# Optimization experiments

Measured on AMD Instinct MI355X. Metric: run time of the kernel, lower is better.

Reference implementation:

```python
import jax, jax.numpy as jnp
import numpy as np

C = 96          # channels (= output_dim)
NUM_HEADS = 6
DILS = (1, 2, 3)
KS_ATT = 3      # dilate-attention kernel size
KS_COR = 5      # self-correlation kernel size
PAD_COR = 2
LN_EPS = 1e-5


def _unfold(x, k, dil, pad):
    # torch.nn.Unfold(kernel=k, dilation=dil, padding=pad, stride=1)
    # x: [B, C, H, W] -> [B, C, k*k, H, W] (channel-major, kernel row-major)
    B, c, H, W = x.shape
    xp = jnp.pad(x, ((0, 0), (0, 0), (pad, pad), (pad, pad)))
    patches = [xp[:, :, i * dil:i * dil + H, j * dil:j * dil + W]
               for i in range(k) for j in range(k)]
    return jnp.stack(patches, axis=2)


def _layernorm(x, g, b):
    m = jnp.mean(x, axis=-1, keepdims=True)
    v = jnp.mean((x - m) ** 2, axis=-1, keepdims=True)
    return (x - m) * jax.lax.rsqrt(v + LN_EPS) * g + b


def _dilate_attn(q, k, v, dil, head_dim, scale):
    # q,k,v: [B, cb, H, W] with cb = C // num_dilation
    B, cb, H, W = q.shape
    heads = cb // head_dim
    qf = q.reshape(B, heads, head_dim, H * W)                                  # bhdn
    kp = _unfold(k, KS_ATT, dil, dil).reshape(B, heads, head_dim, KS_ATT * KS_ATT, H * W)
    attn = jax.nn.softmax(jnp.einsum('bhdn,bhdkn->bhnk', qf, kp) * scale, axis=-1)
    vp = _unfold(v, KS_ATT, dil, dil).reshape(B, heads, head_dim, KS_ATT * KS_ATT, H * W)
    out = jnp.einsum('bhnk,bhdkn->bnhd', attn, vp)                             # [B,HW,heads,hd]
    return out.reshape(B, H, W, cb)


def _forward(x, g1, b1, Wqkv, bqkv, Wproj, bproj, g2, b2, W1, bm1, W2, bm2):
    B, Cc, H, W = x.shape
    nd = len(DILS)
    head_dim = Cc // NUM_HEADS
    scale = head_dim ** (-0.5)

    xh = jnp.transpose(x, (0, 2, 3, 1))                                        # [B,H,W,C]

    # --- MultiDilatelocalAttention block ---
    y = _layernorm(xh, g1, b1)
    qkv = jnp.einsum('bhwc,oc->bhwo', y, Wqkv) + bqkv                          # 1x1 conv == linear
    qkv = jnp.transpose(qkv, (0, 3, 1, 2)).reshape(B, 3, nd, Cc // nd, H, W)
    outs = []
    for i, d in enumerate(DILS):
        outs.append(_dilate_attn(qkv[:, 0, i], qkv[:, 1, i], qkv[:, 2, i], d, head_dim, scale))
    a = jnp.concatenate(outs, axis=-1)                                         # dilation-major channels
    a = a @ Wproj.T + bproj
    xh = xh + a

    # --- MLP block ---
    z = _layernorm(xh, g2, b2)
    z = jax.nn.gelu(z @ W1.T + bm1, approximate=False) @ W2.T + bm2
    xh = xh + z

    # --- self-correlation ---
    xc = jnp.transpose(xh, (0, 3, 1, 2))                                       # [B,C,H,W]
    xc = jax.nn.relu(xc)
    nrm = jnp.sqrt(jnp.sum(xc * xc, axis=1, keepdims=True))
    xc = xc / jnp.maximum(nrm, 1e-12)                                          # F.normalize dim=1
    pat = _unfold(xc, KS_COR, 1, PAD_COR)                                      # [B,C,25,H,W]
    out = pat.reshape(B, Cc, KS_COR, KS_COR, H, W) * xc[:, :, None, None]
    return jnp.transpose(out, (0, 1, 4, 5, 2, 3))                              # [B,C,H,W,5,5]


def setup_inputs() -> dict:
    key = jax.random.key(0)
    ks = jax.random.split(key, 8)
    B, H, W = 8, 64, 64
    s = 0.02
    return {
        'x': jax.random.normal(ks[0], (B, C, H, W), jnp.float32),
        'g1': jnp.ones((C,), jnp.float32),
        'b1': jnp.zeros((C,), jnp.float32),
        'Wqkv': jax.random.normal(ks[1], (3 * C, C), jnp.float32) * s,
        'bqkv': jnp.zeros((3 * C,), jnp.float32),
        'Wproj': jax.random.normal(ks[2], (C, C), jnp.float32) * s,
        'bproj': jnp.zeros((C,), jnp.float32),
        'g2': jnp.ones((C,), jnp.float32),
        'b2': jnp.zeros((C,), jnp.float32),
        'W1': jax.random.normal(ks[3], (4 * C, C), jnp.float32) * s,
        'bm1': jnp.zeros((4 * C,), jnp.float32),
        'W2': jax.random.normal(ks[4], (C, 4 * C), jnp.float32) * s,
        'bm2': jnp.zeros((C,), jnp.float32),
    }


def reference(x, g1, b1, Wqkv, bqkv, Wproj, bproj, g2, b2, W1, bm1, W2, bm2):
    return _forward(x, g1, b1, Wqkv, bqkv, Wproj, bproj, g2, b2, W1, bm1, W2, bm2)
```

## Files before the change

### kernel.cpp

```cpp
#include <hip/hip_runtime.h>
#include <math.h>

#define NN 4096
#define BN 32768

using short8 = __attribute__((ext_vector_type(8))) short;
using f32x4  = __attribute__((ext_vector_type(4))) float;
typedef unsigned short ushort_t;

__device__ inline ushort_t f2bf(float f) {
    unsigned u = __builtin_bit_cast(unsigned, f);
    u += 0x7FFFu + ((u >> 16) & 1u);
    return (ushort_t)(u >> 16);
}
__device__ inline float bflo(unsigned u) {
    return __builtin_bit_cast(float, u << 16);
}
__device__ inline float bfhi(unsigned u) {
    return __builtin_bit_cast(float, u & 0xFFFF0000u);
}
__device__ inline float bf2f(ushort_t h) {
    return __builtin_bit_cast(float, ((unsigned)h) << 16);
}

__global__ __launch_bounds__(256) void k0_cvt(
    const float* __restrict__ Wqkv, const float* __restrict__ Wproj,
    const float* __restrict__ W1, const float* __restrict__ W2,
    ushort_t* __restrict__ wb)
{
    int i = blockIdx.x * 256 + threadIdx.x;
    float v;
    if (i < 27648)      v = Wqkv[i];
    else if (i < 36864) v = Wproj[i - 27648];
    else if (i < 73728) v = W1[i - 36864];
    else                v = W2[i - 73728];
    wb[i] = f2bf(v);
}

__global__ __launch_bounds__(256) void k1_ln_qkv(
    const float* __restrict__ x, const float* __restrict__ g1, const float* __restrict__ b1,
    const ushort_t* __restrict__ wqkv_b, const float* __restrict__ bqkv,
    unsigned* __restrict__ qkvt32)
{
    __shared__ __align__(16) float    Cs[96 * 69];
    __shared__ __align__(16) ushort_t As[64 * 104];
    __shared__ __align__(16) ushort_t Bs[96 * 104];
    const int tid = threadIdx.x;
    const long bn0 = (long)blockIdx.x * 64;
    const int b = (int)(bn0 >> 12);
    const int n0 = (int)(bn0 & 4095);
    const unsigned* wqkv32 = (const unsigned*)wqkv_b;

    for (int i = 0; i < 24; ++i) {
        int idx = i * 256 + tid;
        int c = idx >> 6, p = idx & 63;
        Cs[c * 69 + p] = x[((long)(b * 96 + c) << 12) + n0 + p];
    }
    __syncthreads();
    {
        int p = tid >> 2, part = tid & 3, c0 = part * 24;
        float s = 0.f, ss = 0.f;
        for (int c = c0; c < c0 + 24; ++c) { float v = Cs[c*69 + p]; s += v; ss += v*v; }
        s  += __shfl_xor(s, 1);  s  += __shfl_xor(s, 2);
        ss += __shfl_xor(ss, 1); ss += __shfl_xor(ss, 2);
        float m = s * (1.f/96.f);
        float rstd = rsqrtf(ss * (1.f/96.f) - m*m + 1e-5f);
        for (int c = c0; c < c0 + 24; ++c)
            Cs[c*69 + p] = (Cs[c*69 + p] - m) * rstd * g1[c] + b1[c];
    }
    __syncthreads();
    for (int i = 0; i < 12; ++i) {
        int idx = i * 256 + tid;
        int p = idx / 48, cp = idx % 48;
        unsigned lo = f2bf(Cs[(2*cp  )*69 + p]);
        unsigned hi = f2bf(Cs[(2*cp+1)*69 + p]);
        *(unsigned*)&As[p * 104 + 2*cp] = lo | (hi << 16);
    }

    const int lane = tid & 63, wv = tid >> 6;
    const int ln = lane & 15, qd = lane >> 4;
    for (int ch = 0; ch < 3; ++ch) {
        __syncthreads();
        for (int i = 0; i < 18; ++i) {
            int idx = i * 256 + tid;
            int o = idx / 48, cp = idx % 48;
            *(unsigned*)&Bs[o * 104 + 2*cp] = wqkv32[(ch*96 + o)*48 + cp];
        }
        __syncthreads();
        f32x4 acc[6];
        #pragma unroll
        for (int t = 0; t < 6; ++t) acc[t] = (f32x4){0.f, 0.f, 0.f, 0.f};
        #pragma unroll
        for (int kc = 0; kc < 3; ++kc) {
            short8 a = *(const short8*)&As[(wv*16 + ln)*104 + kc*32 + qd*8];
            #pragma unroll
            for (int t = 0; t < 6; ++t) {
                short8 bf = *(const short8*)&Bs[(t*16 + ln)*104 + kc*32 + qd*8];
                acc[t] = __builtin_amdgcn_mfma_f32_16x16x32_bf16(a, bf, acc[t], 0, 0, 0);
            }
        }
        #pragma unroll
        for (int t = 0; t < 6; ++t)
            #pragma unroll
            for (int r = 0; r < 4; ++r)
                Cs[(t*16 + ln)*69 + (wv*16 + qd*4 + r)] = acc[t][r];
        __syncthreads();
        for (int i = 0; i < 12; ++i) {
            int idx = i * 256 + tid;
            int cp = idx / 64, p = idx % 64;
            int c = 2*cp;
            float b0v = bqkv[ch*96 + c], b1v = bqkv[ch*96 + c + 1];
            unsigned lo = f2bf(Cs[c*69 + p] + b0v);
            unsigned hi = f2bf(Cs[(c+1)*69 + p] + b1v);
            qkvt32[((long)(b*144 + ch*48 + cp) << 12) + n0 + p] = lo | (hi << 16);
        }
    }
}

__global__ __launch_bounds__(256) void k2_attn(
    const unsigned* __restrict__ qkvt32, unsigned* __restrict__ abt32)
{
    int t = blockIdx.x * 256 + threadIdx.x;
    int n = t & 4095;
    int r = t >> 12;
    int head = r & 1;
    int di = (r >> 1) % 3;
    int b = r / 6;
    int h = n >> 6, w = n & 63;
    int dil = di + 1;
    const int cp0 = di*16 + head*8;
    const unsigned* Q = qkvt32 + ((long)(b*144 +      cp0) << 12);
    const unsigned* K = qkvt32 + ((long)(b*144 + 48 + cp0) << 12);
    const unsigned* V = qkvt32 + ((long)(b*144 + 96 + cp0) << 12);

    float q[16];
    #pragma unroll
    for (int j = 0; j < 8; ++j) {
        unsigned u = Q[((long)j << 12) + n];
        q[2*j] = bflo(u); q[2*j+1] = bfhi(u);
    }

    float logits[9];
    #pragma unroll
    for (int ki = 0; ki < 3; ++ki)
        #pragma unroll
        for (int kj = 0; kj < 3; ++kj) {
            int hh = h + (ki-1)*dil, ww = w + (kj-1)*dil;
            float l = 0.f;
            if ((unsigned)hh < 64u && (unsigned)ww < 64u) {
                int nn = (hh << 6) + ww;
                #pragma unroll
                for (int j = 0; j < 8; ++j) {
                    unsigned u = K[((long)j << 12) + nn];
                    l += q[2*j] * bflo(u) + q[2*j+1] * bfhi(u);
                }
            }
            logits[ki*3 + kj] = l * 0.25f;
        }
    float m = logits[0];
    #pragma unroll
    for (int k = 1; k < 9; ++k) m = fmaxf(m, logits[k]);
    float e[9], s = 0.f;
    #pragma unroll
    for (int k = 0; k < 9; ++k) { e[k] = expf(logits[k] - m); s += e[k]; }
    float inv = 1.f / s;

    float o[16];
    #pragma unroll
    for (int d = 0; d < 16; ++d) o[d] = 0.f;
    #pragma unroll
    for (int ki = 0; ki < 3; ++ki)
        #pragma unroll
        for (int kj = 0; kj < 3; ++kj) {
            int hh = h + (ki-1)*dil, ww = w + (kj-1)*dil;
            if ((unsigned)hh < 64u && (unsigned)ww < 64u) {
                int nn = (hh << 6) + ww;
                float wgt = e[ki*3 + kj] * inv;
                #pragma unroll
                for (int j = 0; j < 8; ++j) {
                    unsigned u = V[((long)j << 12) + nn];
                    o[2*j]   += wgt * bflo(u);
                    o[2*j+1] += wgt * bfhi(u);
                }
            }
        }
    #pragma unroll
    for (int j = 0; j < 8; ++j) {
        unsigned lo = f2bf(o[2*j]), hi = f2bf(o[2*j+1]);
        abt32[((long)(b*48 + cp0 + j) << 12) + n] = lo | (hi << 16);
    }
}

__global__ __launch_bounds__(256) void k345(
    const unsigned* __restrict__ abt32, const float* __restrict__ x,
    const ushort_t* __restrict__ wproj_b, const float* __restrict__ bproj,
    const float* __restrict__ g2, const float* __restrict__ b2,
    const ushort_t* __restrict__ w1_b, const float* __restrict__ bm1,
    const ushort_t* __restrict__ w2_b, const float* __restrict__ bm2,
    float* __restrict__ xcn)
{
    __shared__ __align__(16) float    Cs[96 * 69];
    __shared__ __align__(16) ushort_t As[64 * 104];
    __shared__ __align__(16) ushort_t Ah[64 * 104];
    __shared__ __align__(16) ushort_t Bs[96 * 104];
    __shared__ float lnm[64], lnr[64];
    const int tid = threadIdx.x;
    const long bn0 = (long)blockIdx.x * 64;
    const int b = (int)(bn0 >> 12);
    const int n0 = (int)(bn0 & 4095);
    const unsigned* wproj32 = (const unsigned*)wproj_b;
    const unsigned* w1_32   = (const unsigned*)w1_b;
    const unsigned* w2_32   = (const unsigned*)w2_b;
    const int lane = tid & 63, wv = tid >> 6;
    const int ln = lane & 15, qd = lane >> 4;

    for (int i = 0; i < 12; ++i) {
        int idx = i * 256 + tid;
        int cp = idx / 64, p = idx % 64;
        *(unsigned*)&As[p * 104 + 2*cp] = abt32[((long)(b*48 + cp) << 12) + n0 + p];
    }
    for (int i = 0; i < 18; ++i) {
        int idx = i * 256 + tid;
        int o = idx / 48, cp = idx % 48;
        *(unsigned*)&Bs[o * 104 + 2*cp] = wproj32[o*48 + cp];
    }
    __syncthreads();
    {
        f32x4 acc[6];
        #pragma unroll
        for (int t = 0; t < 6; ++t) acc[t] = (f32x4){0.f, 0.f, 0.f, 0.f};
        #pragma unroll
        for (int kc = 0; kc < 3; ++kc) {
            short8 a = *(const short8*)&As[(wv*16 + ln)*104 + kc*32 + qd*8];
            #pragma unroll
            for (int t = 0; t < 6; ++t) {
                short8 bf = *(const short8*)&Bs[(t*16 + ln)*104 + kc*32 + qd*8];
                acc[t] = __builtin_amdgcn_mfma_f32_16x16x32_bf16(a, bf, acc[t], 0, 0, 0);
            }
        }
        #pragma unroll
        for (int t = 0; t < 6; ++t)
            #pragma unroll
            for (int r = 0; r < 4; ++r)
                Cs[(t*16 + ln)*69 + (wv*16 + qd*4 + r)] = acc[t][r];
    }
    __syncthreads();
    float resid[24];
    #pragma unroll
    for (int i = 0; i < 24; ++i) {
        int idx = i * 256 + tid;
        int c = idx >> 6, p = idx & 63;
        float v = Cs[c*69 + p] + bproj[c] + x[((long)(b*96 + c) << 12) + n0 + p];
        resid[i] = v;
        Cs[c*69 + p] = v;
    }
    __syncthreads();
    {
        int p = tid >> 2, part = tid & 3, c0 = part * 24;
        float s = 0.f, ss = 0.f;
        for (int c = c0; c < c0 + 24; ++c) { float v = Cs[c*69 + p]; s += v; ss += v*v; }
        s  += __shfl_xor(s, 1);  s  += __shfl_xor(s, 2);
        ss += __shfl_xor(ss, 1); ss += __shfl_xor(ss, 2);
        float m = s * (1.f/96.f);
        float rstd = rsqrtf(ss * (1.f/96.f) - m*m + 1e-5f);
        if (part == 0) { lnm[p] = m; lnr[p] = rstd; }
    }
    __syncthreads();
    for (int i = 0; i < 12; ++i) {
        int idx = i * 256 + tid;
        int p = idx / 48, cp = idx % 48;
        float m = lnm[p], rs = lnr[p];
        int c = 2*cp;
        unsigned lo = f2bf((Cs[(c  )*69 + p] - m) * rs * g2[c  ] + b2[c  ]);
        unsigned hi = f2bf((Cs[(c+1)*69 + p] - m) * rs * g2[c+1] + b2[c+1]);
        *(unsigned*)&As[p * 104 + 2*cp] = lo | (hi << 16);
    }

    f32x4 acc2[6];
    #pragma unroll
    for (int t = 0; t < 6; ++t) acc2[t] = (f32x4){0.f, 0.f, 0.f, 0.f};
    for (int kb = 0; kb < 4; ++kb) {
        __syncthreads();
        for (int i = 0; i < 18; ++i) {
            int idx = i * 256 + tid;
            int o = idx / 48, cp = idx % 48;
            *(unsigned*)&Bs[o * 104 + 2*cp] = w1_32[(kb*96 + o)*48 + cp];
        }
        __syncthreads();
        f32x4 acch[6];
        #pragma unroll
        for (int t = 0; t < 6; ++t) acch[t] = (f32x4){0.f, 0.f, 0.f, 0.f};
        #pragma unroll
        for (int kc = 0; kc < 3; ++kc) {
            short8 a = *(const short8*)&As[(wv*16 + ln)*104 + kc*32 + qd*8];
            #pragma unroll
            for (int t = 0; t < 6; ++t) {
                short8 bf = *(const short8*)&Bs[(t*16 + ln)*104 + kc*32 + qd*8];
                acch[t] = __builtin_amdgcn_mfma_f32_16x16x32_bf16(a, bf, acch[t], 0, 0, 0);
            }
        }
        #pragma unroll
        for (int t = 0; t < 6; ++t) {
            float bias = bm1[kb*96 + t*16 + ln];
            #pragma unroll
            for (int r = 0; r < 4; ++r) {
                float v = acch[t][r] + bias;
                v = 0.5f * v * (1.f + erff(v * 0.70710678118654752f));
                Ah[(wv*16 + qd*4 + r)*104 + t*16 + ln] = f2bf(v);
            }
        }
        __syncthreads();
        for (int i = 0; i < 18; ++i) {
            int idx = i * 256 + tid;
            int o = idx / 48, cp = idx % 48;
            *(unsigned*)&Bs[o * 104 + 2*cp] = w2_32[o*192 + kb*48 + cp];
        }
        __syncthreads();
        #pragma unroll
        for (int kc = 0; kc < 3; ++kc) {
            short8 a = *(const short8*)&Ah[(wv*16 + ln)*104 + kc*32 + qd*8];
            #pragma unroll
            for (int t = 0; t < 6; ++t) {
                short8 bf = *(const short8*)&Bs[(t*16 + ln)*104 + kc*32 + qd*8];
                acc2[t] = __builtin_amdgcn_mfma_f32_16x16x32_bf16(a, bf, acc2[t], 0, 0, 0);
            }
        }
    }
    __syncthreads();
    #pragma unroll
    for (int t = 0; t < 6; ++t)
        #pragma unroll
        for (int r = 0; r < 4; ++r)
            Cs[(t*16 + ln)*69 + (wv*16 + qd*4 + r)] = acc2[t][r];
    __syncthreads();
    #pragma unroll
    for (int i = 0; i < 24; ++i) {
        int idx = i * 256 + tid;
        int c = idx >> 6, p = idx & 63;
        float v = Cs[c*69 + p] + bm2[c] + resid[i];
        Cs[c*69 + p] = fmaxf(v, 0.f);
    }
    __syncthreads();
    {
        int p = tid >> 2, part = tid & 3, c0 = part * 24;
        float ss = 0.f;
        for (int c = c0; c < c0 + 24; ++c) { float v = Cs[c*69 + p]; ss += v*v; }
        ss += __shfl_xor(ss, 1); ss += __shfl_xor(ss, 2);
        if (part == 0) lnr[p] = 1.f / fmaxf(sqrtf(ss), 1e-12f);
    }
    __syncthreads();
    for (int i = 0; i < 12; ++i) {
        int idx = i * 256 + tid;
        int p = idx / 48, cp = idx % 48;
        float inv = lnr[p];
        float2 v = make_float2(Cs[(2*cp)*69 + p] * inv, Cs[(2*cp+1)*69 + p] * inv);
        *(float2*)&xcn[(bn0 + p) * 96 + 2*cp] = v;
    }
}

__global__ __launch_bounds__(256) void k6_selfcorr(
    const float* __restrict__ xcn, float* __restrict__ out)
{
    __shared__ float xt[5 * 20 * 97];
    const int tid = threadIdx.x;
    const int wc = blockIdx.x;
    const int h  = blockIdx.y;
    const int b  = blockIdx.z;
    const int w0 = wc * 16;

    for (int i = 0; i < 38; ++i) {
        int idx = i * 256 + tid;
        if (idx < 9600) {
            int r = idx / (20 * 96);
            int rem = idx - r * (20 * 96);
            int wi = rem / 96, c = rem - wi * 96;
            int hh = h + r - 2, ww = w0 + wi - 2;
            float v = 0.f;
            if ((unsigned)hh < 64u && (unsigned)ww < 64u)
                v = xcn[(((long)b << 12) + (hh << 6) + ww) * 96 + c];
            xt[(r * 20 + wi) * 97 + c] = v;
        }
    }
    __syncthreads();
    float4* out4 = (float4*)out;
    const long ob4 = (long)b * 2457600 + (long)h * 400 + wc * 100;
    for (int i = 0; i < 38; ++i) {
        int idx = i * 256 + tid;
        if (idx < 9600) {
            int c = idx / 100;
            int r4 = idx - c * 100;
            float4 v;
            #pragma unroll
            for (int j = 0; j < 4; ++j) {
                int r = r4 * 4 + j;
                int lw = r / 25, k = r - lw * 25;
                int ki = k / 5, kj = k - ki * 5;
                float center = xt[(42 + lw) * 97 + c];
                float neigh  = xt[(ki * 20 + lw + kj) * 97 + c];
                (&v.x)[j] = center * neigh;
            }
            out4[ob4 + (long)c * 25600 + r4] = v;
        }
    }
}

extern "C" void kernel_launch(void* const* d_in, const int* in_sizes, int n_in,
                              void* d_out, int out_size, void* d_ws, size_t ws_size,
                              hipStream_t stream)
{
    const float* x     = (const float*)d_in[0];
    const float* g1    = (const float*)d_in[1];
    const float* b1    = (const float*)d_in[2];
    const float* Wqkv  = (const float*)d_in[3];
    const float* bqkv  = (const float*)d_in[4];
    const float* Wproj = (const float*)d_in[5];
    const float* bproj = (const float*)d_in[6];
    const float* g2    = (const float*)d_in[7];
    const float* b2    = (const float*)d_in[8];
    const float* W1    = (const float*)d_in[9];
    const float* bm1   = (const float*)d_in[10];
    const float* W2    = (const float*)d_in[11];
    const float* bm2   = (const float*)d_in[12];
    float* out = (float*)d_out;

    char* w = (char*)d_ws;
    unsigned* qkvt32 = (unsigned*)w;  w += (size_t)BN * 288 * 2;
    unsigned* abt32  = (unsigned*)w;  w += (size_t)BN * 96 * 2;
    float*    xcn    = (float*)w;     w += (size_t)BN * 96 * 4;
    ushort_t* wb     = (ushort_t*)w;  w += (size_t)110592 * 2;
    ushort_t* wqkv_b = wb;
    ushort_t* wproj_b= wb + 27648;
    ushort_t* w1_b   = wb + 36864;
    ushort_t* w2_b   = wb + 73728;

    k0_cvt     <<<432, 256, 0, stream>>>(Wqkv, Wproj, W1, W2, wb);
    k1_ln_qkv  <<<BN / 64, 256, 0, stream>>>(x, g1, b1, wqkv_b, bqkv, qkvt32);
    k2_attn    <<<(BN * 6) / 256, 256, 0, stream>>>(qkvt32, abt32);
    k345       <<<BN / 64, 256, 0, stream>>>(abt32, x, wproj_b, bproj, g2, b2,
                                             w1_b, bm1, w2_b, bm2, xcn);
    k6_selfcorr<<<dim3(4, 64, 8), 256, 0, stream>>>(xcn, out);
}
```

Before: 479.7 us.

## Fuse dilated attention into projection/MLP kernel and convert weights inline

Measured after the change: 436.0 us. -9.1%, faster.

```diff
diff --git a/kernel.cpp b/kernel.cpp
--- a/kernel.cpp
+++ b/kernel.cpp
@@ -8,38 +8,19 @@
 using f32x4  = __attribute__((ext_vector_type(4))) float;
 typedef unsigned short ushort_t;
 
-__device__ inline ushort_t f2bf(float f) {
+__device__ inline unsigned f2bfu(float f) {
     unsigned u = __builtin_bit_cast(unsigned, f);
     u += 0x7FFFu + ((u >> 16) & 1u);
-    return (ushort_t)(u >> 16);
+    return u >> 16;
 }
-__device__ inline float bflo(unsigned u) {
-    return __builtin_bit_cast(float, u << 16);
-}
-__device__ inline float bfhi(unsigned u) {
-    return __builtin_bit_cast(float, u & 0xFFFF0000u);
-}
-__device__ inline float bf2f(ushort_t h) {
-    return __builtin_bit_cast(float, ((unsigned)h) << 16);
-}
-
-__global__ __launch_bounds__(256) void k0_cvt(
-    const float* __restrict__ Wqkv, const float* __restrict__ Wproj,
-    const float* __restrict__ W1, const float* __restrict__ W2,
-    ushort_t* __restrict__ wb)
-{
-    int i = blockIdx.x * 256 + threadIdx.x;
-    float v;
-    if (i < 27648)      v = Wqkv[i];
-    else if (i < 36864) v = Wproj[i - 27648];
-    else if (i < 73728) v = W1[i - 36864];
-    else                v = W2[i - 73728];
-    wb[i] = f2bf(v);
-}
+__device__ inline ushort_t f2bf(float f) { return (ushort_t)f2bfu(f); }
+__device__ inline unsigned pack2(float a, float b) { return f2bfu(a) | (f2bfu(b) << 16); }
+__device__ inline float bflo(unsigned u) { return __builtin_bit_cast(float, u << 16); }
+__device__ inline float bfhi(unsigned u) { return __builtin_bit_cast(float, u & 0xFFFF0000u); }
 
 __global__ __launch_bounds__(256) void k1_ln_qkv(
     const float* __restrict__ x, const float* __restrict__ g1, const float* __restrict__ b1,
-    const ushort_t* __restrict__ wqkv_b, const float* __restrict__ bqkv,
+    const float* __restrict__ Wqkv, const float* __restrict__ bqkv,
     unsigned* __restrict__ qkvt32)
 {
     __shared__ __align__(16) float    Cs[96 * 69];
@@ -49,7 +30,6 @@
     const long bn0 = (long)blockIdx.x * 64;
     const int b = (int)(bn0 >> 12);
     const int n0 = (int)(bn0 & 4095);
-    const unsigned* wqkv32 = (const unsigned*)wqkv_b;
 
     for (int i = 0; i < 24; ++i) {
         int idx = i * 256 + tid;
@@ -72,19 +52,19 @@
     for (int i = 0; i < 12; ++i) {
         int idx = i * 256 + tid;
         int p = idx / 48, cp = idx % 48;
-        unsigned lo = f2bf(Cs[(2*cp  )*69 + p]);
-        unsigned hi = f2bf(Cs[(2*cp+1)*69 + p]);
-        *(unsigned*)&As[p * 104 + 2*cp] = lo | (hi << 16);
+        *(unsigned*)&As[p * 104 + 2*cp] = pack2(Cs[(2*cp)*69 + p], Cs[(2*cp+1)*69 + p]);
     }
 
     const int lane = tid & 63, wv = tid >> 6;
     const int ln = lane & 15, qd = lane >> 4;
     for (int ch = 0; ch < 3; ++ch) {
         __syncthreads();
-        for (int i = 0; i < 18; ++i) {
+        for (int i = 0; i < 9; ++i) {
             int idx = i * 256 + tid;
-            int o = idx / 48, cp = idx % 48;
-            *(unsigned*)&Bs[o * 104 + 2*cp] = wqkv32[(ch*96 + o)*48 + cp];
+            int o = idx / 24, q4 = idx % 24;
+            float4 wvv = *(const float4*)&Wqkv[(long)(ch*96 + o)*96 + q4*4];
+            uint2 d; d.x = pack2(wvv.x, wvv.y); d.y = pack2(wvv.z, wvv.w);
+            *(uint2*)&Bs[o * 104 + q4*4] = d;
         }
         __syncthreads();
         f32x4 acc[6];
@@ -109,94 +89,19 @@
             int idx = i * 256 + tid;
             int cp = idx / 64, p = idx % 64;
             int c = 2*cp;
-            float b0v = bqkv[ch*96 + c], b1v = bqkv[ch*96 + c + 1];
-            unsigned lo = f2bf(Cs[c*69 + p] + b0v);
-            unsigned hi = f2bf(Cs[(c+1)*69 + p] + b1v);
-            qkvt32[((long)(b*144 + ch*48 + cp) << 12) + n0 + p] = lo | (hi << 16);
+            unsigned d = pack2(Cs[c*69 + p] + bqkv[ch*96 + c],
+                               Cs[(c+1)*69 + p] + bqkv[ch*96 + c + 1]);
+            qkvt32[((long)(b*144 + ch*48 + cp) << 12) + n0 + p] = d;
         }
     }
 }
 
-__global__ __launch_bounds__(256) void k2_attn(
-    const unsigned* __restrict__ qkvt32, unsigned* __restrict__ abt32)
-{
-    int t = blockIdx.x * 256 + threadIdx.x;
-    int n = t & 4095;
-    int r = t >> 12;
-    int head = r & 1;
-    int di = (r >> 1) % 3;
-    int b = r / 6;
-    int h = n >> 6, w = n & 63;
-    int dil = di + 1;
-    const int cp0 = di*16 + head*8;
-    const unsigned* Q = qkvt32 + ((long)(b*144 +      cp0) << 12);
-    const unsigned* K = qkvt32 + ((long)(b*144 + 48 + cp0) << 12);
-    const unsigned* V = qkvt32 + ((long)(b*144 + 96 + cp0) << 12);
-
-    float q[16];
-    #pragma unroll
-    for (int j = 0; j < 8; ++j) {
-        unsigned u = Q[((long)j << 12) + n];
-        q[2*j] = bflo(u); q[2*j+1] = bfhi(u);
-    }
-
-    float logits[9];
-    #pragma unroll
-    for (int ki = 0; ki < 3; ++ki)
-        #pragma unroll
-        for (int kj = 0; kj < 3; ++kj) {
-            int hh = h + (ki-1)*dil, ww = w + (kj-1)*dil;
-            float l = 0.f;
-            if ((unsigned)hh < 64u && (unsigned)ww < 64u) {
-                int nn = (hh << 6) + ww;
-                #pragma unroll
-                for (int j = 0; j < 8; ++j) {
-                    unsigned u = K[((long)j << 12) + nn];
-                    l += q[2*j] * bflo(u) + q[2*j+1] * bfhi(u);
-                }
-            }
-            logits[ki*3 + kj] = l * 0.25f;
-        }
-    float m = logits[0];
-    #pragma unroll
-    for (int k = 1; k < 9; ++k) m = fmaxf(m, logits[k]);
-    float e[9], s = 0.f;
-    #pragma unroll
-    for (int k = 0; k < 9; ++k) { e[k] = expf(logits[k] - m); s += e[k]; }
-    float inv = 1.f / s;
-
-    float o[16];
-    #pragma unroll
-    for (int d = 0; d < 16; ++d) o[d] = 0.f;
-    #pragma unroll
-    for (int ki = 0; ki < 3; ++ki)
-        #pragma unroll
-        for (int kj = 0; kj < 3; ++kj) {
-            int hh = h + (ki-1)*dil, ww = w + (kj-1)*dil;
-            if ((unsigned)hh < 64u && (unsigned)ww < 64u) {
-                int nn = (hh << 6) + ww;
-                float wgt = e[ki*3 + kj] * inv;
-                #pragma unroll
-                for (int j = 0; j < 8; ++j) {
-                    unsigned u = V[((long)j << 12) + nn];
-                    o[2*j]   += wgt * bflo(u);
-                    o[2*j+1] += wgt * bfhi(u);
-                }
-            }
-        }
-    #pragma unroll
-    for (int j = 0; j < 8; ++j) {
-        unsigned lo = f2bf(o[2*j]), hi = f2bf(o[2*j+1]);
-        abt32[((long)(b*48 + cp0 + j) << 12) + n] = lo | (hi << 16);
-    }
-}
-
-__global__ __launch_bounds__(256) void k345(
-    const unsigned* __restrict__ abt32, const float* __restrict__ x,
-    const ushort_t* __restrict__ wproj_b, const float* __restrict__ bproj,
+__global__ __launch_bounds__(256) void k2345(
+    const unsigned* __restrict__ qkvt32, const float* __restrict__ x,
+    const float* __restrict__ Wproj, const float* __restrict__ bproj,
     const float* __restrict__ g2, const float* __restrict__ b2,
-    const ushort_t* __restrict__ w1_b, const float* __restrict__ bm1,
-    const ushort_t* __restrict__ w2_b, const float* __restrict__ bm2,
+    const float* __restrict__ W1, const float* __restrict__ bm1,
+    const float* __restrict__ W2, const float* __restrict__ bm2,
     float* __restrict__ xcn)
 {
     __shared__ __align__(16) float    Cs[96 * 69];
@@ -208,21 +113,83 @@
     const long bn0 = (long)blockIdx.x * 64;
     const int b = (int)(bn0 >> 12);
     const int n0 = (int)(bn0 & 4095);
-    const unsigned* wproj32 = (const unsigned*)wproj_b;
-    const unsigned* w1_32   = (const unsigned*)w1_b;
-    const unsigned* w2_32   = (const unsigned*)w2_b;
+    const int h0 = n0 >> 6;
     const int lane = tid & 63, wv = tid >> 6;
     const int ln = lane & 15, qd = lane >> 4;
 
-    for (int i = 0; i < 12; ++i) {
-        int idx = i * 256 + tid;
-        int cp = idx / 64, p = idx % 64;
-        *(unsigned*)&As[p * 104 + 2*cp] = abt32[((long)(b*48 + cp) << 12) + n0 + p];
-    }
-    for (int i = 0; i < 18; ++i) {
-        int idx = i * 256 + tid;
-        int o = idx / 48, cp = idx % 48;
-        *(unsigned*)&Bs[o * 104 + 2*cp] = wproj32[o*48 + cp];
+    for (int it = 0; it < 2; ++it) {
+        int item = it * 256 + tid;
+        if (item < 384) {
+            int p = item & 63;
+            int r = item >> 6;
+            int head = r & 1, di = r >> 1;
+            int dil = di + 1;
+            int cp0 = di*16 + head*8;
+            const unsigned* Q = qkvt32 + ((long)(b*144 +      cp0) << 12);
+            const unsigned* K = qkvt32 + ((long)(b*144 + 48 + cp0) << 12);
+            const unsigned* V = qkvt32 + ((long)(b*144 + 96 + cp0) << 12);
+            int n = n0 + p, w = p;
+
+            float q[16];
+            #pragma unroll
+            for (int j = 0; j < 8; ++j) {
+                unsigned u = Q[((long)j << 12) + n];
+                q[2*j] = bflo(u); q[2*j+1] = bfhi(u);
+            }
+            float logits[9];
+            #pragma unroll
+            for (int ki = 0; ki < 3; ++ki)
+                #pragma unroll
+                for (int kj = 0; kj < 3; ++kj) {
+                    int hh = h0 + (ki-1)*dil, ww = w + (kj-1)*dil;
+                    float l = 0.f;
+                    if ((unsigned)hh < 64u && (unsigned)ww < 64u) {
+                        int nn = (hh << 6) + ww;
+                        #pragma unroll
+                        for (int j = 0; j < 8; ++j) {
+                            unsigned u = K[((long)j << 12) + nn];
+                            l += q[2*j] * bflo(u) + q[2*j+1] * bfhi(u);
+                        }
+                    }
+                    logits[ki*3 + kj] = l * 0.25f;
+                }
+            float m = logits[0];
+            #pragma unroll
+            for (int k = 1; k < 9; ++k) m = fmaxf(m, logits[k]);
+            float e[9], s = 0.f;
+            #pragma unroll
+            for (int k = 0; k < 9; ++k) { e[k] = expf(logits[k] - m); s += e[k]; }
+            float inv = 1.f / s;
+            float o[16];
+            #pragma unroll
+            for (int d = 0; d < 16; ++d) o[d] = 0.f;
+            #pragma unroll
+            for (int ki = 0; ki < 3; ++ki)
+                #pragma unroll
+                for (int kj = 0; kj < 3; ++kj) {
+                    int hh = h0 + (ki-1)*dil, ww = w + (kj-1)*dil;
+                    if ((unsigned)hh < 64u && (unsigned)ww < 64u) {
+                        int nn = (hh << 6) + ww;
+                        float wgt = e[ki*3 + kj] * inv;
+                        #pragma unroll
+                        for (int j = 0; j < 8; ++j) {
+                            unsigned u = V[((long)j << 12) + nn];
+                            o[2*j]   += wgt * bflo(u);
+                            o[2*j+1] += wgt * bfhi(u);
+                        }
+                    }
+                }
+            #pragma unroll
+            for (int j = 0; j < 8; ++j)
+                *(unsigned*)&As[p * 104 + 2*(cp0 + j)] = pack2(o[2*j], o[2*j+1]);
+        }
+    }
+    for (int i = 0; i < 9; ++i) {
+        int idx = i * 256 + tid;
+        int o = idx / 24, q4 = idx % 24;
+        float4 wvv = *(const float4*)&Wproj[(long)o*96 + q4*4];
+        uint2 d; d.x = pack2(wvv.x, wvv.y); d.y = pack2(wvv.z, wvv.w);
+        *(uint2*)&Bs[o * 104 + q4*4] = d;
     }
     __syncthreads();
     {
@@ -271,20 +238,21 @@
         int p = idx / 48, cp = idx % 48;
         float m = lnm[p], rs = lnr[p];
         int c = 2*cp;
-        unsigned lo = f2bf((Cs[(c  )*69 + p] - m) * rs * g2[c  ] + b2[c  ]);
-        unsigned hi = f2bf((Cs[(c+1)*69 + p] - m) * rs * g2[c+1] + b2[c+1]);
-        *(unsigned*)&As[p * 104 + 2*cp] = lo | (hi << 16);
-    }
-
+        unsigned d = pack2((Cs[(c  )*69 + p] - m) * rs * g2[c  ] + b2[c  ],
+                           (Cs[(c+1)*69 + p] - m) * rs * g2[c+1] + b2[c+1]);
+        *(unsigned*)&As[p * 104 + 2*cp] = d;
+    }
     f32x4 acc2[6];
     #pragma unroll
     for (int t = 0; t < 6; ++t) acc2[t] = (f32x4){0.f, 0.f, 0.f, 0.f};
     for (int kb = 0; kb < 4; ++kb) {
         __syncthreads();
-        for (int i = 0; i < 18; ++i) {
+        for (int i = 0; i < 9; ++i) {
             int idx = i * 256 + tid;
-            int o = idx / 48, cp = idx % 48;
-            *(unsigned*)&Bs[o * 104 + 2*cp] = w1_32[(kb*96 + o)*48 + cp];
+            int o = idx / 24, q4 = idx % 24;
+            float4 wvv = *(const float4*)&W1[(long)(kb*96 + o)*96 + q4*4];
+            uint2 d; d.x = pack2(wvv.x, wvv.y); d.y = pack2(wvv.z, wvv.w);
+            *(uint2*)&Bs[o * 104 + q4*4] = d;
         }
         __syncthreads();
         f32x4 acch[6];
@@ -310,10 +278,12 @@
             }
         }
         __syncthreads();
-        for (int i = 0; i < 18; ++i) {
+        for (int i = 0; i < 9; ++i) {
             int idx = i * 256 + tid;
-            int o = idx / 48, cp = idx % 48;
-            *(unsigned*)&Bs[o * 104 + 2*cp] = w2_32[o*192 + kb*48 + cp];
+            int o = idx / 24, q4 = idx % 24;
+            float4 wvv = *(const float4*)&W2[(long)o*384 + kb*96 + q4*4];
+            uint2 d; d.x = pack2(wvv.x, wvv.y); d.y = pack2(wvv.z, wvv.w);
+            *(uint2*)&Bs[o * 104 + q4*4] = d;
         }
         __syncthreads();
         #pragma unroll
@@ -382,14 +352,14 @@
         }
     }
     __syncthreads();
-    float4* out4 = (float4*)out;
+    f32x4* out4 = (f32x4*)out;
     const long ob4 = (long)b * 2457600 + (long)h * 400 + wc * 100;
     for (int i = 0; i < 38; ++i) {
         int idx = i * 256 + tid;
         if (idx < 9600) {
             int c = idx / 100;
             int r4 = idx - c * 100;
-            float4 v;
+            f32x4 v;
             #pragma unroll
             for (int j = 0; j < 4; ++j) {
                 int r = r4 * 4 + j;
@@ -397,9 +367,9 @@
                 int ki = k / 5, kj = k - ki * 5;
                 float center = xt[(42 + lw) * 97 + c];
                 float neigh  = xt[(ki * 20 + lw + kj) * 97 + c];
-                (&v.x)[j] = center * neigh;
-            }
-            out4[ob4 + (long)c * 25600 + r4] = v;
+                v[j] = center * neigh;
+            }
+            __builtin_nontemporal_store(v, &out4[ob4 + (long)c * 25600 + r4]);
         }
     }
 }
@@ -425,18 +395,10 @@
 
     char* w = (char*)d_ws;
     unsigned* qkvt32 = (unsigned*)w;  w += (size_t)BN * 288 * 2;
-    unsigned* abt32  = (unsigned*)w;  w += (size_t)BN * 96 * 2;
-    float*    xcn    = (float*)w;     w += (size_t)BN * 96 * 4;
-    ushort_t* wb     = (ushort_t*)w;  w += (size_t)110592 * 2;
-    ushort_t* wqkv_b = wb;
-    ushort_t* wproj_b= wb + 27648;
-    ushort_t* w1_b   = wb + 36864;
-    ushort_t* w2_b   = wb + 73728;
-
-    k0_cvt     <<<432, 256, 0, stream>>>(Wqkv, Wproj, W1, W2, wb);
-    k1_ln_qkv  <<<BN / 64, 256, 0, stream>>>(x, g1, b1, wqkv_b, bqkv, qkvt32);
-    k2_attn    <<<(BN * 6) / 256, 256, 0, stream>>>(qkvt32, abt32);
-    k345       <<<BN / 64, 256, 0, stream>>>(abt32, x, wproj_b, bproj, g2, b2,
-                                             w1_b, bm1, w2_b, bm2, xcn);
+    float*    xcn    = (float*)w;
+
+    k1_ln_qkv  <<<BN / 64, 256, 0, stream>>>(x, g1, b1, Wqkv, bqkv, qkvt32);
+    k2345      <<<BN / 64, 256, 0, stream>>>(qkvt32, x, Wproj, bproj, g2, b2,
+                                             W1, bm1, W2, bm2, xcn);
     k6_selfcorr<<<dim3(4, 64, 8), 256, 0, stream>>>(xcn, out);
 }
```
